# Performance work log

Hardware: AMD Instinct MI355X
Metric: run time of the kernel (lower is better)

Reference implementation:

```python
import jax, jax.numpy as jnp
import numpy as np

DIM = 1024
NUM_HEADS = 1  # module's proj-after-squeeze only type-checks with 1 head
HEAD_DIM = DIM // NUM_HEADS
NQ = 8192
NK = 8192
B = 1


def setup_inputs() -> dict:
    key = jax.random.key(0)
    ks = jax.random.split(key, 12)
    s = 0.02  # weight init scale
    return {
        "q": jax.random.normal(ks[0], (NQ, B, DIM), jnp.float32),
        "k": jax.random.normal(ks[1], (NK, B, DIM), jnp.float32),
        "v": jax.random.normal(ks[2], (NK, B, DIM), jnp.float32),
        "ref_boxes": jax.random.uniform(ks[3], (NK, B, 4), jnp.float32),
        "query_boxes": jax.random.uniform(ks[4], (NQ, B, 4), jnp.float32),
        "Wq": jax.random.normal(ks[5], (DIM, DIM), jnp.float32) * s,
        "Wk": jax.random.normal(ks[6], (DIM, DIM), jnp.float32) * s,
        "Wv": jax.random.normal(ks[7], (DIM, DIM), jnp.float32) * s,
        "Wp": jax.random.normal(ks[8], (DIM, DIM), jnp.float32) * s,
        "bp": jnp.zeros((DIM,), jnp.float32),
        "W1": jax.random.normal(ks[9], (DIM, 2 * DIM), jnp.float32) * s,
        "b1": jnp.zeros((2 * DIM,), jnp.float32),
        "W2": jax.random.normal(ks[10], (2 * DIM, NUM_HEADS), jnp.float32) * s,
        "b2": jnp.zeros((NUM_HEADS,), jnp.float32),
    }


def _centers(boxes):  # [N, B, 4] -> [B, N, 2]
    c = (boxes[..., :2] + boxes[..., 2:]) * 0.5
    return jnp.transpose(c, (1, 0, 2))


def reference(q, k, v, ref_boxes, query_boxes, Wq, Wk, Wv, Wp, bp, W1, b1, W2, b2):
    Nq, Bsz, dim = q.shape
    Nk = k.shape[0]
    H = W2.shape[1]
    hd = dim // H
    scale = hd ** -0.5

    # bias_weight = sigmoid(MLP(var(k, dim=0)))  -- torch.var is unbiased (ddof=1)
    gfv = jnp.var(k, axis=0, ddof=1)                       # [B, dim]
    bias_weight = jax.nn.sigmoid(
        jax.nn.relu(gfv @ W1 + b1) @ W2 + b2
    )                                                       # [B, H]

    # seq-first -> batch-first, project, split heads
    qb = jnp.transpose(q, (1, 0, 2))                        # [B, Nq, dim]
    kb = jnp.transpose(k, (1, 0, 2))
    vb = jnp.transpose(v, (1, 0, 2))
    qh = (qb @ Wq).reshape(Bsz, Nq, H, hd).transpose(0, 2, 1, 3) * scale
    kh = (kb @ Wk).reshape(Bsz, Nk, H, hd).transpose(0, 2, 1, 3)
    vh = (vb @ Wv).reshape(Bsz, Nk, H, hd).transpose(0, 2, 1, 3)

    attn = jnp.einsum('bhqd,bhkd->bhqk', qh, kh)            # [B, H, Nq, Nk]

    # relative-position bias: per-head learned weight * (-pairwise box-center distance)
    cq = _centers(query_boxes)                              # [B, Nq, 2]
    cr = _centers(ref_boxes)                                # [B, Nk, 2]
    d2 = jnp.sum((cq[:, :, None, :] - cr[:, None, :, :]) ** 2, axis=-1)
    dist = jnp.sqrt(d2 + 1e-8)                              # [B, Nq, Nk]
    attn = attn - bias_weight[:, :, None, None] * dist[:, None, :, :]

    attn = jax.nn.softmax(attn, axis=-1)
    x = jnp.einsum('bhqk,bhkd->bhqd', attn, vh)             # [B, H, Nq, hd]
    x = jnp.squeeze(x)                                      # [Nq, dim] since B=H=1
    return x @ Wp + bp
```

## Files before the change

kernel.cpp:

```cpp
#include <hip/hip_runtime.h>
#include <math.h>

#define DIM 1024
#define NQ 8192
#define NK 8192

typedef unsigned short u16;
typedef __attribute__((ext_vector_type(8))) short short8;
typedef __attribute__((ext_vector_type(8))) u16 u16x8;
typedef __attribute__((ext_vector_type(4))) u16 u16x4;
typedef __attribute__((ext_vector_type(4))) float f32x4;
typedef __attribute__((address_space(1))) const unsigned int gu32;
typedef __attribute__((address_space(3))) unsigned int lu32;

__device__ inline u16 f2bf(float f) {
  unsigned u = __builtin_bit_cast(unsigned, f);
  u += 0x7fff + ((u >> 16) & 1);
  return (u16)(u >> 16);
}
__device__ inline float bf2f(u16 h) {
  unsigned u = ((unsigned)h) << 16;
  return __builtin_bit_cast(float, u);
}


__global__ void var_partial_kernel(const float* __restrict__ k,
                                   float* __restrict__ ps, float* __restrict__ pq) {
  int col = blockIdx.x * 256 + threadIdx.x;
  int r0  = blockIdx.y * 256;
  float s = 0.f, q = 0.f;
  for (int r = 0; r < 256; ++r) {
    float x = k[(size_t)(r0 + r) * DIM + col];
    s += x; q += x * x;
  }
  ps[blockIdx.y * DIM + col] = s;
  pq[blockIdx.y * DIM + col] = q;
}

__global__ void gfv_kernel(const float* __restrict__ ps, const float* __restrict__ pq,
                           float* __restrict__ gfv) {
  int col = blockIdx.x * 256 + threadIdx.x;
  float s = 0.f, q = 0.f;
  for (int c = 0; c < 32; ++c) { s += ps[c * DIM + col]; q += pq[c * DIM + col]; }
  const float n = 8192.f;
  gfv[col] = (q - s * s / n) / (n - 1.f);
}

__global__ void h1_partial_kernel(const float* __restrict__ gfv, const float* __restrict__ W1,
                                  float* __restrict__ h1p) {
  int j  = blockIdx.x * 256 + threadIdx.x;
  int d0 = blockIdx.y * 128;
  float acc = 0.f;
  for (int d = 0; d < 128; ++d)
    acc += gfv[d0 + d] * W1[(size_t)(d0 + d) * 2048 + j];
  h1p[blockIdx.y * 2048 + j] = acc;
}

__global__ void bw_kernel(const float* __restrict__ h1p, const float* __restrict__ b1,
                          const float* __restrict__ W2, const float* __restrict__ b2,
                          float* __restrict__ bw) {
  __shared__ float red[256];
  int t = threadIdx.x;
  float acc = 0.f;
  for (int i = 0; i < 8; ++i) {
    int j = i * 256 + t;
    float h = b1[j];
    for (int c = 0; c < 8; ++c) h += h1p[c * 2048 + j];
    h = fmaxf(h, 0.f);
    acc += h * W2[j];
  }
  red[t] = acc; __syncthreads();
  for (int s = 128; s > 0; s >>= 1) { if (t < s) red[t] += red[t + s]; __syncthreads(); }
  if (t == 0) bw[0] = 1.f / (1.f + __expf(-(red[0] + b2[0])));
}

__global__ void centers_kernel(const float4* __restrict__ qb, const float4* __restrict__ rb,
                               float2* __restrict__ cq, float2* __restrict__ cr) {
  int i = blockIdx.x * 256 + threadIdx.x;
  float4 a = qb[i];
  cq[i] = make_float2(0.5f * (a.x + a.z), 0.5f * (a.y + a.w));
  float4 b = rb[i];
  cr[i] = make_float2(0.5f * (b.x + b.z), 0.5f * (b.y + b.w));
}


__global__ void f2bf3_kernel(const float4* __restrict__ a, const float4* __restrict__ b,
                             const float4* __restrict__ c, u16x4* __restrict__ oa,
                             u16x4* __restrict__ ob, u16x4* __restrict__ oc, int n4) {
  const float4* in = (blockIdx.y == 0) ? a : (blockIdx.y == 1) ? b : c;
  u16x4* out = (blockIdx.y == 0) ? oa : (blockIdx.y == 1) ? ob : oc;
  for (int i = blockIdx.x * 256 + threadIdx.x; i < n4; i += gridDim.x * 256) {
    float4 v = in[i];
    u16x4 o;
    o[0] = f2bf(v.x); o[1] = f2bf(v.y); o[2] = f2bf(v.z); o[3] = f2bf(v.w);
    out[i] = o;
  }
}

__global__ __launch_bounds__(256) void wtrans4_kernel(
    const float* __restrict__ W0, const float* __restrict__ W1,
    const float* __restrict__ W2, const float* __restrict__ W3,
    u16* __restrict__ T0, u16* __restrict__ T1, u16* __restrict__ T2, u16* __restrict__ T3) {
  const float* W = (blockIdx.z == 0) ? W0 : (blockIdx.z == 1) ? W1 : (blockIdx.z == 2) ? W2 : W3;
  u16* WT = (blockIdx.z == 0) ? T0 : (blockIdx.z == 1) ? T1 : (blockIdx.z == 2) ? T2 : T3;
  __shared__ float tile[64][65];
  const int t = threadIdx.x;
  const int kb = blockIdx.x * 64, nb = blockIdx.y * 64;
#pragma unroll
  for (int i = 0; i < 16; ++i) {
    int r = i * 4 + (t >> 6), c = t & 63;
    tile[c][r] = W[(size_t)(kb + r) * 1024 + nb + c];
  }
  __syncthreads();
#pragma unroll
  for (int i = 0; i < 16; ++i) {
    int n = i * 4 + (t >> 6), kk = t & 63;
    WT[(size_t)(nb + n) * 1024 + kb + kk] = f2bf(tile[n][kk]);
  }
}


#define TM 128
#define TN 128
#define TK 32

template <int OUT>
__global__ __launch_bounds__(256) void bgemm_kernel(
    const u16* __restrict__ A, const u16* __restrict__ Bt, void* __restrict__ C,
    const float* __restrict__ bias, int M, int N, int K, int ldc, float alpha) {
  __shared__ __align__(16) u16 As[TM * TK];
  __shared__ __align__(16) u16 Bs[TN * TK];

  const int t = threadIdx.x;
  const int l = t & 63;
  const int w = t >> 6;
  const int wm = w >> 1, wn = w & 1;
  const size_t row0 = (size_t)blockIdx.y * TM;
  const size_t col0 = (size_t)blockIdx.x * TN;

  f32x4 acc[4][4];
#pragma unroll
  for (int m = 0; m < 4; ++m)
#pragma unroll
    for (int n = 0; n < 4; ++n) acc[m][n] = (f32x4){0.f, 0.f, 0.f, 0.f};

  const int lane_r = l & 15;
  const int kgrp = (l >> 4) * 8;

  for (int k0 = 0; k0 < K; k0 += TK) {
#pragma unroll
    for (int j = 0; j < 2; ++j) {
      int idx = j * 256 + t;
      int r = idx >> 2, c8 = (idx & 3) << 3;
      __builtin_amdgcn_global_load_lds((gu32*)(A + (row0 + r) * K + k0 + c8),
                                       (lu32*)(As + idx * 8), 16, 0, 0);
      __builtin_amdgcn_global_load_lds((gu32*)(Bt + (col0 + r) * K + k0 + c8),
                                       (lu32*)(Bs + idx * 8), 16, 0, 0);
    }
    __syncthreads();

    short8 a[4], b[4];
#pragma unroll
    for (int m = 0; m < 4; ++m)
      a[m] = *(const short8*)&As[(wm * 64 + m * 16 + lane_r) * TK + kgrp];
#pragma unroll
    for (int n = 0; n < 4; ++n)
      b[n] = *(const short8*)&Bs[(wn * 64 + n * 16 + lane_r) * TK + kgrp];
#pragma unroll
    for (int m = 0; m < 4; ++m)
#pragma unroll
      for (int n = 0; n < 4; ++n)
        acc[m][n] = __builtin_amdgcn_mfma_f32_16x16x32_bf16(a[m], b[n], acc[m][n], 0, 0, 0);
    __syncthreads();
  }

#pragma unroll
  for (int m = 0; m < 4; ++m) {
#pragma unroll
    for (int n = 0; n < 4; ++n) {
      size_t col = col0 + wn * 64 + n * 16 + lane_r;
      size_t rbase = row0 + wm * 64 + m * 16 + (l >> 4) * 4;
      if (OUT == 0) {
        float bv = bias[col];
#pragma unroll
        for (int j = 0; j < 4; ++j)
          ((float*)C)[(rbase + j) * (size_t)ldc + col] = acc[m][n][j] * alpha + bv;
      } else if (OUT == 1) {
#pragma unroll
        for (int j = 0; j < 4; ++j)
          ((u16*)C)[(rbase + j) * (size_t)ldc + col] = f2bf(acc[m][n][j] * alpha);
      } else {
        u16x4 p;
#pragma unroll
        for (int j = 0; j < 4; ++j) p[j] = f2bf(acc[m][n][j] * alpha);
        *(u16x4*)&((u16*)C)[col * (size_t)ldc + rbase] = p;
      }
    }
  }
}


template <int VM>
__device__ __forceinline__ void waitvm() {
  if constexpr (VM == 4) asm volatile("s_waitcnt vmcnt(4)" ::: "memory");
  else asm volatile("s_waitcnt vmcnt(0)" ::: "memory");
}
#define FENCE asm volatile("" ::: "memory")
#define BARRIER do { FENCE; __builtin_amdgcn_s_barrier(); FENCE; } while (0)

#define SGA(UNIT, KT, BUF)                                                          \
  __builtin_amdgcn_global_load_lds(                                                 \
      (gu32*)(Agp + (size_t)((UNIT) * 64) * ldaB + (size_t)(KT) * 128),             \
      (lu32*)(smem + (BUF) * 16384 + (UNIT) * 4096 + tid * 8), 16, 0, 0)

#define SGB(UNIT, KT, BUF)                                                          \
  do {                                                                              \
    int _rp = (UNIT) * 64 + rr;                                                     \
    size_t _row = (size_t)(bn0 + ((_rp >> 5) & 3) * 64 + (_rp >> 7) * 32 + (_rp & 31)); \
    __builtin_amdgcn_global_load_lds(                                               \
        (gu32*)(Bgp + _row * ldbB + (size_t)(KT) * 128),                            \
        (lu32*)(smem + 32768 + (BUF) * 16384 + (UNIT) * 4096 + tid * 8), 16, 0, 0); \
  } while (0)

#define RDA4(DST, BO, MQ, KO)                                                       \
  _Pragma("unroll") for (int fr = 0; fr < 4; ++fr)                                  \
    DST[fr] = *(const short8*)(smemc + (BO) + aRd + (MQ) * 8192 + fr * 2048 + (KO));

#define RDB2(NQ_, KK, BO, KO)                                                       \
  _Pragma("unroll") for (int fc = 0; fc < 2; ++fc)                                  \
    bf[NQ_][KK][fc] = *(const short8*)(smemc + 65536 + (BO) + bRd + (NQ_) * 16384 + fc * 2048 + (KO));

#define MM8(AF, MQ, NQ_, KK)                                                        \
  do {                                                                              \
    __builtin_amdgcn_s_setprio(1);                                                  \
    _Pragma("unroll") for (int fr = 0; fr < 4; ++fr)                                \
    _Pragma("unroll") for (int fc = 0; fc < 2; ++fc)                                \
      acc[(MQ) * 4 + fr][(NQ_) * 2 + fc] = __builtin_amdgcn_mfma_f32_16x16x32_bf16( \
          AF[fr], bf[NQ_][KK][fc], acc[(MQ) * 4 + fr][(NQ_) * 2 + fc], 0, 0, 0);    \
    __builtin_amdgcn_s_setprio(0);                                                  \
  } while (0)

template <int OUT>
__global__ __launch_bounds__(512, 2) void gemm256_kernel(
    const u16* __restrict__ A, const u16* __restrict__ Bt, void* __restrict__ C,
    const float* __restrict__ bias, int NT, int nTn, int tmb,
    size_t ldaB, size_t ldbB, int ldc, size_t kspanB, size_t cstride, float alpha) {
  __shared__ __align__(16) u16 smem[65536];
  const char* smemc = (const char*)smem;

  const int tid = threadIdx.x;
  const int l = tid & 63;
  const int wid = tid >> 6;
  const int wm = wid >> 2, wn = wid & 3;
  const int lane_r = l & 15;
  const int kq = l >> 4;
  const int rr = tid >> 3;

  const int bid = blockIdx.x;
  const int xcd = bid & 7;
  const int c = bid >> 3;
  const int tm = xcd * tmb + (c % tmb);
  const int tn = c / tmb;
  const int am0 = tm * 256, bn0 = tn * 256;
  const size_t kglob = kspanB * blockIdx.y;

  int band = 0;
  if (OUT == 2) { band = am0 >> 13; Bt += (size_t)band << 20; }

  const int kx = (lane_r & 7) << 4;
  const int koff0 = (kq << 4) ^ kx;
  const int koff1 = (64 | (kq << 4)) ^ kx;
  const int aRd = (wm * 128 + lane_r) * 128;
  const int bRd = (wn * 32 + lane_r) * 128;

  const int scol = ((tid & 7) ^ ((tid >> 3) & 7)) << 4;
  const char* Agp = (const char*)A + (size_t)(am0 + rr) * ldaB + kglob + scol;
  const char* Bgp = (const char*)Bt + kglob + scol;

  f32x4 acc[8][4];
#pragma unroll
  for (int i = 0; i < 8; ++i)
#pragma unroll
    for (int j = 0; j < 4; ++j) acc[i][j] = (f32x4){0.f, 0.f, 0.f, 0.f};

  short8 afP[4], afQ[4], bf[2][2][2];

  SGA(0, 0, 0); SGA(2, 0, 0); SGB(0, 0, 0); SGB(1, 0, 0);
  SGB(2, 0, 0); SGB(3, 0, 0); SGA(1, 0, 0); SGA(3, 0, 0);
  waitvm<0>();
  BARRIER;
  RDA4(afP, 0, 0, koff0);
  RDB2(0, 0, 0, koff0);

  for (int t = 0; t < NT; ++t) {
    const int bo = (t & 1) * 32768;
    const int nbo = bo ^ 32768;
    const int nb = (t & 1) ^ 1;
    const bool more = (t + 1 < NT);
    if (more) { SGA(0, t + 1, nb); SGA(2, t + 1, nb); }
    RDB2(1, 0, bo, koff0);
    MM8(afP, 0, 0, 0);
    if (more) { SGB(0, t + 1, nb); SGB(1, t + 1, nb); }
    RDA4(afQ, bo, 1, koff0);
    MM8(afP, 0, 1, 0);
    if (more) { SGB(2, t + 1, nb); SGB(3, t + 1, nb); }
    RDB2(0, 1, bo, koff1);
    MM8(afQ, 1, 1, 0);
    if (more) { SGA(1, t + 1, nb); SGA(3, t + 1, nb); }
    RDA4(afP, bo, 1, koff1);
    MM8(afQ, 1, 0, 0);
    RDB2(1, 1, bo, koff1);
    MM8(afP, 1, 0, 1);
    RDA4(afQ, bo, 0, koff1);
    MM8(afP, 1, 1, 1);
    MM8(afQ, 0, 1, 1);
    waitvm<4>();
    BARRIER;
    if (more) { RDA4(afP, nbo, 0, koff0); RDB2(0, 0, nbo, koff0); }
    MM8(afQ, 0, 0, 1);
    waitvm<0>();
    BARRIER;
  }

#pragma unroll
  for (int fp = 0; fp < 8; ++fp) {
#pragma unroll
    for (int fc2 = 0; fc2 < 4; ++fc2) {
      int row = am0 + wm * 128 + fp * 16 + kq * 4;
      int col = bn0 + wn * 64 + fc2 * 16 + lane_r;
      if (OUT == 0) {
#pragma unroll
        for (int j = 0; j < 4; ++j)
          ((u16*)C)[(size_t)(row + j) * ldc + col] = f2bf(acc[fp][fc2][j] * alpha);
      } else if (OUT == 1) {
        u16* Cp = (u16*)C + cstride * blockIdx.y;
#pragma unroll
        for (int j = 0; j < 4; ++j)
          Cp[(size_t)(row + j) * ldc + col] = f2bf(acc[fp][fc2][j]);
      } else if (OUT == 3) {
        float* Cf = (float*)C;
        float bv = bias[col];
#pragma unroll
        for (int j = 0; j < 4; ++j)
          Cf[(size_t)(row + j) * ldc + col] = acc[fp][fc2][j] * alpha + bv;
      } else {
        int arow = row & 8191;
        if (band < 2) {
          u16* D = (u16*)C + ((size_t)band << 23);
          float a2 = (band == 0) ? 0.03125f : 1.f;
#pragma unroll
          for (int j = 0; j < 4; ++j)
            D[(size_t)(arow + j) * DIM + col] = f2bf(acc[fp][fc2][j] * a2);
        } else {
          u16* D = (u16*)C + ((size_t)2 << 23);
          u16x4 pk;
#pragma unroll
          for (int j = 0; j < 4; ++j) pk[j] = f2bf(acc[fp][fc2][j]);
          *(u16x4*)&D[(size_t)col * NK + arow] = pk;
        }
      }
    }
  }
}


__global__ void combine4_kernel(const u16x8* __restrict__ p, u16x8* __restrict__ out) {
  const size_t st = (size_t)NQ * DIM / 8;
  size_t i = (size_t)blockIdx.x * 256 + threadIdx.x;
  u16x8 a = p[i], b = p[i + st], c = p[i + 2 * st], d = p[i + 3 * st];
  u16x8 o;
#pragma unroll
  for (int j = 0; j < 8; ++j)
    o[j] = f2bf(bf2f(a[j]) + bf2f(b[j]) + bf2f(c[j]) + bf2f(d[j]));
  out[i] = o;
}


__global__ __launch_bounds__(256) void softmax_bias_bf16_kernel(
    u16* __restrict__ S, const float2* __restrict__ cq, const float2* __restrict__ cr,
    const float* __restrict__ bwp, int qr0) {
  __shared__ float red[256];
  const int t = threadIdx.x;
  u16* row = S + (size_t)blockIdx.x * NK;
  const float2 cqv = cq[qr0 + blockIdx.x];
  const float bw = bwp[0];

  float l[32];
  float mx = -1e30f;
#pragma unroll
  for (int i = 0; i < 4; ++i) {
    int base = (i * 256 + t) * 8;
    u16x8 u = *(const u16x8*)&row[base];
#pragma unroll
    for (int j = 0; j < 8; ++j) {
      float x = bf2f(u[j]);
      float2 c = cr[base + j];
      float dx = cqv.x - c.x, dy = cqv.y - c.y;
      float lv = x - bw * sqrtf(dx * dx + dy * dy + 1e-8f);
      l[i * 8 + j] = lv;
      mx = fmaxf(mx, lv);
    }
  }
  red[t] = mx; __syncthreads();
  for (int s = 128; s > 0; s >>= 1) { if (t < s) red[t] = fmaxf(red[t], red[t + s]); __syncthreads(); }
  mx = red[0]; __syncthreads();

  float sum = 0.f;
#pragma unroll
  for (int i = 0; i < 32; ++i) { float e = __expf(l[i] - mx); l[i] = e; sum += e; }
  red[t] = sum; __syncthreads();
  for (int s = 128; s > 0; s >>= 1) { if (t < s) red[t] += red[t + s]; __syncthreads(); }
  float inv = 1.f / red[0];

#pragma unroll
  for (int i = 0; i < 4; ++i) {
    int base = (i * 256 + t) * 8;
    u16x8 o;
#pragma unroll
    for (int j = 0; j < 8; ++j) o[j] = f2bf(l[i * 8 + j] * inv);
    *(u16x8*)&row[base] = o;
  }
}


extern "C" void kernel_launch(void* const* d_in, const int* in_sizes, int n_in,
                              void* d_out, int out_size, void* d_ws, size_t ws_size,
                              hipStream_t stream) {
  const float* q  = (const float*)d_in[0];
  const float* k  = (const float*)d_in[1];
  const float* v  = (const float*)d_in[2];
  const float* rb = (const float*)d_in[3];
  const float* qb = (const float*)d_in[4];
  const float* Wq = (const float*)d_in[5];
  const float* Wk = (const float*)d_in[6];
  const float* Wv = (const float*)d_in[7];
  const float* Wp = (const float*)d_in[8];
  const float* bp = (const float*)d_in[9];
  const float* W1 = (const float*)d_in[10];
  const float* b1 = (const float*)d_in[11];
  const float* W2 = (const float*)d_in[12];
  const float* b2 = (const float*)d_in[13];
  float* out = (float*)d_out;

  char* p = (char*)d_ws;
  const size_t PROJB = (size_t)NQ * DIM * sizeof(u16);
  u16* qbf = (u16*)p;            p += PROJB;
  u16* kbf = (u16*)p;            p += PROJB;
  u16* vbf = (u16*)p;            p += PROJB;
  u16* qh  = (u16*)p;            p += PROJB;
  u16* kh  = (u16*)p;            p += PROJB;
  u16* vhT = (u16*)p;            p += PROJB;
  u16* WqT = (u16*)p;            p += (size_t)DIM * DIM * 2;
  u16* WkT = (u16*)p;            p += (size_t)DIM * DIM * 2;
  u16* WvT = (u16*)p;            p += (size_t)DIM * DIM * 2;
  u16* WpT = (u16*)p;            p += (size_t)DIM * DIM * 2;
  float* cq  = (float*)p;        p += 2 * NQ * 4;
  float* cr  = (float*)p;        p += 2 * NK * 4;
  float* ps  = (float*)p;        p += 32 * DIM * 4;
  float* pq  = (float*)p;        p += 32 * DIM * 4;
  float* gfv = (float*)p;        p += DIM * 4;
  float* h1p = (float*)p;        p += 8 * 2048 * 4;
  float* bw  = (float*)p;        p += 64;
  size_t fixed_b = (size_t)(p - (char*)d_ws);

  int SR = 256;
  for (int cand = 8192; cand >= 256; cand >>= 1) {
    if (fixed_b + (size_t)cand * (NK + DIM) * 2 <= ws_size) { SR = cand; break; }
  }
  u16* Sbuf = (u16*)p;
  u16* Obuf = Sbuf + (size_t)SR * NK;

  var_partial_kernel<<<dim3(4, 32), 256, 0, stream>>>(k, ps, pq);
  gfv_kernel<<<4, 256, 0, stream>>>(ps, pq, gfv);
  h1_partial_kernel<<<dim3(8, 8), 256, 0, stream>>>(gfv, W1, h1p);
  bw_kernel<<<1, 256, 0, stream>>>(h1p, b1, W2, b2, bw);
  centers_kernel<<<32, 256, 0, stream>>>((const float4*)qb, (const float4*)rb,
                                         (float2*)cq, (float2*)cr);

  const int N4 = NQ * DIM / 4;
  f2bf3_kernel<<<dim3(1024, 3), 256, 0, stream>>>(
      (const float4*)q, (const float4*)k, (const float4*)v,
      (u16x4*)qbf, (u16x4*)kbf, (u16x4*)vbf, N4);
  wtrans4_kernel<<<dim3(16, 16, 4), 256, 0, stream>>>(Wq, Wk, Wv, Wp, WqT, WkT, WvT, WpT);

  gemm256_kernel<2><<<dim3(384, 1), 512, 0, stream>>>(
      qbf, WqT, qh, nullptr, 16, 4, 12, 2048, 2048, DIM, 0, 0, 1.f);

  if (SR == 8192) {
    gemm256_kernel<0><<<dim3(1024, 1), 512, 0, stream>>>(
        qh, kh, Sbuf, nullptr, 16, 32, 4, 2048, 2048, NK, 0, 0, 1.f);
    softmax_bias_bf16_kernel<<<8192, 256, 0, stream>>>(
        Sbuf, (const float2*)cq, (const float2*)cr, bw, 0);
    gemm256_kernel<1><<<dim3(128, 4), 512, 0, stream>>>(
        Sbuf, vhT, qbf, nullptr, 32, 4, 4, 16384, 16384, DIM, 4096, (size_t)NQ * DIM, 1.f);
    combine4_kernel<<<4096, 256, 0, stream>>>((const u16x8*)qbf, (u16x8*)Obuf);
    gemm256_kernel<3><<<dim3(128, 1), 512, 0, stream>>>(
        Obuf, WpT, out, bp, 16, 4, 4, 2048, 2048, DIM, 0, 0, 1.f);
  } else {
    for (int s0 = 0; s0 < NQ; s0 += SR) {
      bgemm_kernel<1><<<dim3(NK / TN, SR / TM), 256, 0, stream>>>(
          qh + (size_t)s0 * DIM, kh, Sbuf, nullptr, SR, NK, DIM, NK, 1.f);
      softmax_bias_bf16_kernel<<<SR, 256, 0, stream>>>(
          Sbuf, (const float2*)cq, (const float2*)cr, bw, s0);
      bgemm_kernel<1><<<dim3(DIM / TN, SR / TM), 256, 0, stream>>>(
          Sbuf, vhT, Obuf, nullptr, SR, DIM, NK, DIM, 1.f);
      bgemm_kernel<0><<<dim3(DIM / TN, SR / TM), 256, 0, stream>>>(
          Obuf, WpT, out + (size_t)s0 * DIM, bp, SR, DIM, DIM, DIM, 1.f);
    }
  }
}
```

Before: 467.7 us.

## Fuse bias, exp and row-sum into QK^T GEMM epilogue, defer normalization

```diff
diff --git a/kernel.cpp b/kernel.cpp
--- a/kernel.cpp
+++ b/kernel.cpp
@@ -243,7 +243,9 @@
 template <int OUT>
 __global__ __launch_bounds__(512, 2) void gemm256_kernel(
     const u16* __restrict__ A, const u16* __restrict__ Bt, void* __restrict__ C,
-    const float* __restrict__ bias, int NT, int nTn, int tmb,
+    const float* __restrict__ bias, const float2* __restrict__ cqp,
+    const float2* __restrict__ crp, const float* __restrict__ bwp,
+    float* __restrict__ psum, int NT, int nTn, int tmb,
     size_t ldaB, size_t ldbB, int ldc, size_t kspanB, size_t cstride, float alpha) {
   __shared__ __align__(16) u16 smem[65536];
   const char* smemc = (const char*)smem;
@@ -322,6 +324,44 @@
     BARRIER;
   }
 
+  if (OUT == 4) {
+    const float bw = bwp[0];
+    float* psld = (float*)smem;
+    float2 crv[4];
+#pragma unroll
+    for (int fc2 = 0; fc2 < 4; ++fc2) crv[fc2] = crp[bn0 + wn * 64 + fc2 * 16 + lane_r];
+#pragma unroll
+    for (int fp = 0; fp < 8; ++fp) {
+      float rs[4] = {0.f, 0.f, 0.f, 0.f};
+      int rbase = am0 + wm * 128 + fp * 16 + kq * 4;
+#pragma unroll
+      for (int j = 0; j < 4; ++j) {
+        float2 cqv = cqp[rbase + j];
+#pragma unroll
+        for (int fc2 = 0; fc2 < 4; ++fc2) {
+          float dx = cqv.x - crv[fc2].x, dy = cqv.y - crv[fc2].y;
+          float pv = __expf(acc[fp][fc2][j] - bw * sqrtf(dx * dx + dy * dy + 1e-8f));
+          rs[j] += pv;
+          int col = bn0 + wn * 64 + fc2 * 16 + lane_r;
+          ((u16*)C)[(size_t)(rbase + j) * ldc + col] = f2bf(pv);
+        }
+      }
+#pragma unroll
+      for (int j = 0; j < 4; ++j) {
+        float s = rs[j];
+        s += __shfl_xor(s, 1); s += __shfl_xor(s, 2);
+        s += __shfl_xor(s, 4); s += __shfl_xor(s, 8);
+        if (lane_r == 0)
+          psld[(wm * 128 + fp * 16 + kq * 4 + j) * 4 + wn] = s;
+      }
+    }
+    __syncthreads();
+    if (tid < 256) {
+      float s = psld[tid * 4] + psld[tid * 4 + 1] + psld[tid * 4 + 2] + psld[tid * 4 + 3];
+      psum[(size_t)tn * NQ + am0 + tid] = s;
+    }
+    return;
+  }
 #pragma unroll
   for (int fp = 0; fp < 8; ++fp) {
 #pragma unroll
@@ -364,14 +404,25 @@
 }
 
 
-__global__ void combine4_kernel(const u16x8* __restrict__ p, u16x8* __restrict__ out) {
+__global__ void rowinv_kernel(const float* __restrict__ psum, float* __restrict__ inv) {
+  int r = blockIdx.x * 256 + threadIdx.x;
+  float s = 0.f;
+#pragma unroll
+  for (int t = 0; t < 32; ++t) s += psum[(size_t)t * NQ + r];
+  inv[r] = 1.f / s;
+}
+
+
+__global__ void combine4_kernel(const u16x8* __restrict__ p, const float* __restrict__ inv,
+                                u16x8* __restrict__ out) {
   const size_t st = (size_t)NQ * DIM / 8;
   size_t i = (size_t)blockIdx.x * 256 + threadIdx.x;
   u16x8 a = p[i], b = p[i + st], c = p[i + 2 * st], d = p[i + 3 * st];
+  float iv = inv[i >> 7];
   u16x8 o;
 #pragma unroll
   for (int j = 0; j < 8; ++j)
-    o[j] = f2bf(bf2f(a[j]) + bf2f(b[j]) + bf2f(c[j]) + bf2f(d[j]));
+    o[j] = f2bf((bf2f(a[j]) + bf2f(b[j]) + bf2f(c[j]) + bf2f(d[j])) * iv);
   out[i] = o;
 }
 
@@ -461,6 +512,8 @@
   float* gfv = (float*)p;        p += DIM * 4;
   float* h1p = (float*)p;        p += 8 * 2048 * 4;
   float* bw  = (float*)p;        p += 64;
+  float* psum = (float*)p;       p += (size_t)32 * NQ * 4;
+  float* rinv = (float*)p;       p += (size_t)NQ * 4;
   size_t fixed_b = (size_t)(p - (char*)d_ws);
 
   int SR = 256;
@@ -484,18 +537,21 @@
   wtrans4_kernel<<<dim3(16, 16, 4), 256, 0, stream>>>(Wq, Wk, Wv, Wp, WqT, WkT, WvT, WpT);
 
   gemm256_kernel<2><<<dim3(384, 1), 512, 0, stream>>>(
-      qbf, WqT, qh, nullptr, 16, 4, 12, 2048, 2048, DIM, 0, 0, 1.f);
+      qbf, WqT, qh, nullptr, nullptr, nullptr, nullptr, nullptr,
+      16, 4, 12, 2048, 2048, DIM, 0, 0, 1.f);
 
   if (SR == 8192) {
-    gemm256_kernel<0><<<dim3(1024, 1), 512, 0, stream>>>(
-        qh, kh, Sbuf, nullptr, 16, 32, 4, 2048, 2048, NK, 0, 0, 1.f);
-    softmax_bias_bf16_kernel<<<8192, 256, 0, stream>>>(
-        Sbuf, (const float2*)cq, (const float2*)cr, bw, 0);
+    gemm256_kernel<4><<<dim3(1024, 1), 512, 0, stream>>>(
+        qh, kh, Sbuf, nullptr, (const float2*)cq, (const float2*)cr, bw, psum,
+        16, 32, 4, 2048, 2048, NK, 0, 0, 1.f);
+    rowinv_kernel<<<32, 256, 0, stream>>>(psum, rinv);
     gemm256_kernel<1><<<dim3(128, 4), 512, 0, stream>>>(
-        Sbuf, vhT, qbf, nullptr, 32, 4, 4, 16384, 16384, DIM, 4096, (size_t)NQ * DIM, 1.f);
-    combine4_kernel<<<4096, 256, 0, stream>>>((const u16x8*)qbf, (u16x8*)Obuf);
+        Sbuf, vhT, qbf, nullptr, nullptr, nullptr, nullptr, nullptr,
+        32, 4, 4, 16384, 16384, DIM, 4096, (size_t)NQ * DIM, 1.f);
+    combine4_kernel<<<4096, 256, 0, stream>>>((const u16x8*)qbf, rinv, (u16x8*)Obuf);
     gemm256_kernel<3><<<dim3(128, 1), 512, 0, stream>>>(
-        Obuf, WpT, out, bp, 16, 4, 4, 2048, 2048, DIM, 0, 0, 1.f);
+        Obuf, WpT, out, bp, nullptr, nullptr, nullptr, nullptr,
+        16, 4, 4, 2048, 2048, DIM, 0, 0, 1.f);
   } else {
     for (int s0 = 0; s0 < NQ; s0 += SR) {
       bgemm_kernel<1><<<dim3(NK / TN, SR / TM), 256, 0, stream>>>(
```

Measured after the change: 465.0 us. About the same (-0.6%).
